# Performance work log

Measured on AMD Instinct MI355X. Metric: run time of the kernel, lower is better.

Reference implementation:

```python
import jax, jax.numpy as jnp
import numpy as np

N = 50000          # nodes
E = 800000         # edges (before self loops)
F_IN = 16
HID = 64
HEADS = 4
C = 64             # per-head out channels (concat=False)
G = 64             # graphs in batch
NEG_SLOPE = 0.2


def setup_inputs() -> dict:
    key = jax.random.key(0)
    ks = jax.random.split(key, 20)
    inp = {
        "x": jax.random.normal(ks[0], (N, F_IN), jnp.float32),
        "edge_index": jax.random.randint(ks[1], (2, E), 0, N, jnp.int64),
        "batch": jnp.sort(jax.random.randint(ks[2], (N,), 0, G, jnp.int64)),
        "W_in": jax.random.normal(ks[3], (HID, F_IN), jnp.float32) * 0.1,
        "b_in": jnp.zeros((HID,), jnp.float32),
        "W_out": jax.random.normal(ks[4], (1, HID), jnp.float32) * 0.1,
        "b_out": jnp.zeros((1,), jnp.float32),
    }
    for l in range(3):
        inp[f"W{l}"] = jax.random.normal(ks[5 + 4 * l], (HEADS * C, HID), jnp.float32) * 0.1
        inp[f"asrc{l}"] = jax.random.normal(ks[6 + 4 * l], (HEADS, C), jnp.float32) * 0.1
        inp[f"adst{l}"] = jax.random.normal(ks[7 + 4 * l], (HEADS, C), jnp.float32) * 0.1
        inp[f"bg{l}"] = jnp.zeros((HID,), jnp.float32)
    return inp


def _gat_layer(x, W, a_src, a_dst, bias, src, dst, n):
    # x: [N, HID] -> h: [N, HEADS, C]
    h = (x @ W.T).reshape(n, HEADS, C)
    alpha_s = jnp.einsum("nhc,hc->nh", h, a_src)   # [N, H]
    alpha_d = jnp.einsum("nhc,hc->nh", h, a_dst)
    e = jax.nn.leaky_relu(alpha_s[src] + alpha_d[dst], NEG_SLOPE)  # [E', H]
    # segment softmax over incoming edges of each dst node
    m = jax.ops.segment_max(e, dst, num_segments=n)
    e = jnp.exp(e - m[dst])
    s = jax.ops.segment_sum(e, dst, num_segments=n)
    alpha = e / (s[dst] + 1e-16)                                   # [E', H]
    msg = alpha[:, :, None] * h[src]                               # [E', H, C]
    out = jax.ops.segment_sum(msg, dst, num_segments=n)            # [N, H, C]
    return out.mean(axis=1) + bias                                 # concat=False: head mean


def reference(x, W_in, b_in, W0, asrc0, adst0, bg0, W1, asrc1, adst1, bg1,
              W2, asrc2, adst2, bg2, W_out, b_out, edge_index, batch):
    n = x.shape[0]
    # add self loops (PyG GATConv default)
    loops = jnp.arange(n, dtype=edge_index.dtype)
    src = jnp.concatenate([edge_index[0], loops])
    dst = jnp.concatenate([edge_index[1], loops])

    h = x @ W_in.T + b_in
    for W, a_s, a_d, bg in ((W0, asrc0, adst0, bg0),
                            (W1, asrc1, adst1, bg1),
                            (W2, asrc2, adst2, bg2)):
        h = jax.nn.relu(_gat_layer(h, W, a_s, a_d, bg, src, dst, n))
        # dropout p=0.2 is inactive in eval mode

    # global mean pool over graphs
    sums = jax.ops.segment_sum(h, batch, num_segments=G)
    cnt = jax.ops.segment_sum(jnp.ones((n,), h.dtype), batch, num_segments=G)
    graph_emb = sums / jnp.maximum(cnt, 1.0)[:, None]              # [G, HID]

    return jax.nn.sigmoid(graph_emb @ W_out.T + b_out)             # [G, 1]
```

## Files before the change

kernel.cpp:

```cpp
#include <hip/hip_runtime.h>
#include <hip/hip_bf16.h>
#include <hip/hip_fp16.h>

#define HID 64
#define HEADS 4
#define GCNT 64
#define F_IN 16
#define NEG 0.2f
#define NBUCK 256
#define BSLOT 6144
#define SCHUNK 2048
#define BSTRIDE 16

typedef _Float16 f16x8 __attribute__((ext_vector_type(8)));
typedef float f32x4 __attribute__((ext_vector_type(4)));

__device__ __forceinline__ unsigned pack_h2(float a, float b) {
  __half2 h = __floats2half2_rn(a, b);
  union { __half2 h; unsigned u; } c;
  c.h = h;
  return c.u;
}
__device__ __forceinline__ __half2 uas_h2(unsigned u) {
  union { unsigned u; __half2 h; } c;
  c.u = u;
  return c.h;
}
__device__ __forceinline__ unsigned h2_as_u(__half2 h) {
  union { __half2 h; unsigned u; } c;
  c.h = h;
  return c.u;
}
__device__ __forceinline__ __half2 xor16_add(__half2 v) {
  unsigned u = (unsigned)__shfl_xor((int)h2_as_u(v), 16, 64);
  return __hadd2(v, uas_h2(u));
}

__global__ __launch_bounds__(256) void k_pre(
    const float* __restrict__ W0, const float* __restrict__ asrc,
    const float* __restrict__ adst, const float* __restrict__ Win,
    const float* __restrict__ bin, int* __restrict__ bcur,
    float* __restrict__ vb, float* __restrict__ c8) {
  int t = threadIdx.x;
  if (blockIdx.x == 0) {
    for (int i = t; i < NBUCK * BSTRIDE; i += 256) bcur[i] = 0;
    return;
  }
  __shared__ float vaL[512];
#pragma unroll
  for (int it = 0; it < 2; ++it) {
    int idx = t + it * 256;
    int q = idx >> 6, j = idx & 63;
    const float* a = (q < 4) ? asrc : adst;
    int h = q & 3;
    float s = 0.f;
    for (int c = 0; c < 64; ++c) s += a[h * 64 + c] * W0[(h * 64 + c) * 64 + j];
    vaL[idx] = s;
  }
  __syncthreads();
  if (t < 128) {
    int q = t >> 4, k = t & 15;
    float s = 0.f;
    for (int j = 0; j < 64; ++j) s += vaL[q * 64 + j] * Win[j * F_IN + k];
    vb[t] = s;
  } else if (t < 136) {
    int q = t - 128;
    float s = 0.f;
    for (int j = 0; j < 64; ++j) s += vaL[q * 64 + j] * bin[j];
    c8[q] = s;
  }
}

__global__ __launch_bounds__(256) void k_binit(
    const int* __restrict__ ei, int* __restrict__ bcur,
    unsigned* __restrict__ tmp, int E, int N,
    const float* __restrict__ x, const float* __restrict__ Win,
    const float* __restrict__ bin,
    const float* __restrict__ W0, const float* __restrict__ W1,
    const float* __restrict__ W2,
    __half* __restrict__ Wh3, __half* __restrict__ Wcat3,
    float* __restrict__ sums, const float* __restrict__ vb,
    const float* __restrict__ c8,
    float* __restrict__ as_, float* __restrict__ ad_,
    __half* __restrict__ hh, int BUK) {
  int t = threadIdx.x;
  if (blockIdx.x < BUK) {
    __shared__ int hist[NBUCK];
    __shared__ int base[NBUCK];
    int start = blockIdx.x * SCHUNK;
    int end = min(start + SCHUNK, E + N);
    hist[t] = 0;
    __syncthreads();
    unsigned val[8];
    int rank[8];
    bool ok[8];
#pragma unroll
    for (int k = 0; k < 8; ++k) {
      int i = start + t + k * 256;
      ok[k] = i < end;
      if (ok[k]) {
        int s, d;
        if (i < E) {
          s = ei[i];
          d = ei[E + i];
        } else {
          s = d = i - E;
        }
        val[k] = ((unsigned)d << 16) | (unsigned)s;
        rank[k] = atomicAdd(&hist[d >> 8], 1);
      }
    }
    __syncthreads();
    int h = hist[t];
    base[t] = h ? atomicAdd(&bcur[t * BSTRIDE], h) : 0;
    __syncthreads();
#pragma unroll
    for (int k = 0; k < 8; ++k) {
      if (ok[k]) {
        int bk = (int)(val[k] >> 24);
        int idx = base[bk] + rank[k];
        if (idx < BSLOT) tmp[(size_t)bk * BSLOT + idx] = val[k];
      }
    }
    return;
  }
  int b = blockIdx.x - BUK;
  if (b < 384) {
    int i = b * 256 + t;
    if (i < 49152) {
      const float* W = (i < 16384) ? W0 : (i < 32768) ? W1 : W2;
      Wh3[i] = __float2half(W[i & 16383]);
    } else {
      int j = i - 49152;
      int l = j >> 14;
      int r = j & 16383;
      int c = r >> 8;
      int k256 = r & 255;
      int h = k256 & 3, kk = k256 >> 2;
      const float* W = (l == 0) ? W0 : (l == 1) ? W1 : W2;
      Wcat3[j] = __float2half(0.25f * W[(h * 64 + c) * 64 + kk]);
    }
    return;
  }
  if (b < 401) {
    int i = (b - 384) * 256 + t;
    if (i < GCNT * HID + GCNT) sums[i] = 0.f;
    return;
  }
  {
    __shared__ float Ws[1024];
    __shared__ float vbs[128];
    __shared__ float bins[64];
    __shared__ float c8s[8];
    for (int i = t; i < 1024; i += 256) Ws[i] = Win[i];
    if (t < 128) vbs[t] = vb[t];
    if (t < 64) bins[t] = bin[t];
    if (t < 8) c8s[t] = c8[t];
    __syncthreads();
    int b2 = b - 401;
    int n = b2 * 64 + (t >> 2);
    int p = t & 3;
    if (n >= N) return;
    const float4* xr4 = (const float4*)(x + (size_t)n * F_IN);
    float4 a0 = xr4[0], a1 = xr4[1], a2 = xr4[2], a3 = xr4[3];
    float xv[16] = {a0.x, a0.y, a0.z, a0.w, a1.x, a1.y, a1.z, a1.w,
                    a2.x, a2.y, a2.z, a2.w, a3.x, a3.y, a3.z, a3.w};
    unsigned hv[8];
#pragma unroll
    for (int jj = 0; jj < 16; jj += 2) {
      int j = p * 16 + jj;
      float acc0 = bins[j], acc1 = bins[j + 1];
#pragma unroll
      for (int k = 0; k < 16; ++k) {
        acc0 = fmaf(xv[k], Ws[j * 16 + k], acc0);
        acc1 = fmaf(xv[k], Ws[(j + 1) * 16 + k], acc1);
      }
      hv[jj >> 1] = pack_h2(acc0, acc1);
    }
    uint4* dst = (uint4*)(hh + (size_t)n * 64 + p * 16);
    dst[0] = make_uint4(hv[0], hv[1], hv[2], hv[3]);
    dst[1] = make_uint4(hv[4], hv[5], hv[6], hv[7]);
    if (p == 0) {
      float sq[8];
#pragma unroll
      for (int q = 0; q < 8; ++q) {
        float s = c8s[q];
#pragma unroll
        for (int k = 0; k < 16; ++k) s = fmaf(xv[k], vbs[q * 16 + k], s);
        sq[q] = s;
      }
      *(float4*)(as_ + (size_t)n * 4) = make_float4(sq[0], sq[1], sq[2], sq[3]);
      *(float4*)(ad_ + (size_t)n * 4) = make_float4(sq[4], sq[5], sq[6], sq[7]);
    }
  }
}

__global__ __launch_bounds__(256) void k_bsort(
    const unsigned* __restrict__ tmp, const int* __restrict__ bcur,
    int* __restrict__ rowptr, int* __restrict__ col, int N) {
  __shared__ int s[NBUCK];
  __shared__ int hist[NBUCK];
  __shared__ int pref[NBUCK];
  int b = blockIdx.x, t = threadIdx.x;
  int c = min(bcur[t * BSTRIDE], BSLOT);
  s[t] = c;
  __syncthreads();
  for (int o = 1; o < 256; o <<= 1) {
    int x = (t >= o) ? s[t - o] : 0;
    __syncthreads();
    s[t] += x;
    __syncthreads();
  }
  int base = (b == 0) ? 0 : s[b - 1];
  int total = s[255];
  int cntb = min(bcur[b * BSTRIDE], BSLOT);
  hist[t] = 0;
  __syncthreads();
  for (int j = t; j < cntb; j += 256)
    atomicAdd(&hist[(tmp[(size_t)b * BSLOT + j] >> 16) & 255], 1);
  __syncthreads();
  int v = hist[t];
  pref[t] = v;
  __syncthreads();
  for (int o = 1; o < 256; o <<= 1) {
    int x = (t >= o) ? pref[t - o] : 0;
    __syncthreads();
    pref[t] += x;
    __syncthreads();
  }
  pref[t] -= v;
  __syncthreads();
  int node = b * 256 + t;
  if (node < N) rowptr[node] = base + pref[t];
  if (b == 255 && t == 255) rowptr[N] = total;
  hist[t] = 0;
  __syncthreads();
  for (int j = t; j < cntb; j += 256) {
    unsigned e = tmp[(size_t)b * BSLOT + j];
    int d8 = (int)((e >> 16) & 255);
    int r = atomicAdd(&hist[d8], 1);
    col[base + pref[d8] + r] = (int)(e & 0xffffu);
  }
}

__device__ __forceinline__ void gat_one_node(
    int node, int lane, const __half* __restrict__ h, const float* __restrict__ as_,
    const float* __restrict__ ad_, const int* __restrict__ rowptr,
    const int* __restrict__ col, __half* __restrict__ Mrow) {
  int r0 = rowptr[node];
  int deg = rowptr[node + 1] - r0;
  float4 adv = *(const float4*)(ad_ + (size_t)node * 4);

  if (deg <= 64) {
    int off = 0;
    float x0 = 0.f, x1 = 0.f, x2 = 0.f, x3 = 0.f;
    if (lane < deg) {
      int s = col[r0 + lane];
      off = s << 6;
      float4 av = *(const float4*)(as_ + (size_t)s * 4);
      float e0 = av.x + adv.x; e0 = (e0 > 0.f) ? e0 : NEG * e0;
      float e1 = av.y + adv.y; e1 = (e1 > 0.f) ? e1 : NEG * e1;
      float e2 = av.z + adv.z; e2 = (e2 > 0.f) ? e2 : NEG * e2;
      float e3 = av.w + adv.w; e3 = (e3 > 0.f) ? e3 : NEG * e3;
      x0 = __expf(fminf(e0, 60.f));
      x1 = __expf(fminf(e1, 60.f));
      x2 = __expf(fminf(e2, 60.f));
      x3 = __expf(fminf(e3, 60.f));
    }
    float s0 = x0, s1 = x1, s2 = x2, s3 = x3;
#pragma unroll
    for (int o = 32; o; o >>= 1) {
      s0 += __shfl_xor(s0, o, 64);
      s1 += __shfl_xor(s1, o, 64);
      s2 += __shfl_xor(s2, o, 64);
      s3 += __shfl_xor(s3, o, 64);
    }
    unsigned w01 = pack_h2(x0 / (s0 + 1e-16f), x1 / (s1 + 1e-16f));
    unsigned w23 = pack_h2(x2 / (s2 + 1e-16f), x3 / (s3 + 1e-16f));
    __half2 acc01 = __floats2half2_rn(0.f, 0.f);
    __half2 acc23 = acc01;
#pragma unroll 4
    for (int j = 0; j < deg; ++j) {
      int oj = __builtin_amdgcn_readlane(off, j) + lane;
      unsigned W01 = __builtin_amdgcn_readlane(w01, j);
      unsigned W23 = __builtin_amdgcn_readlane(w23, j);
      __half2 hv = __half2half2(h[oj]);
      acc01 = __hfma2(hv, uas_h2(W01), acc01);
      acc23 = __hfma2(hv, uas_h2(W23), acc23);
    }
    *(__half2*)&Mrow[lane * 4] = acc01;
    *(__half2*)&Mrow[lane * 4 + 2] = acc23;
    return;
  }
  float m0 = -1e30f, m1 = -1e30f, m2 = -1e30f, m3 = -1e30f;
  for (int j = lane; j < deg; j += 64) {
    int s = col[r0 + j];
    float4 av = *(const float4*)(as_ + (size_t)s * 4);
    float e0 = av.x + adv.x; e0 = (e0 > 0.f) ? e0 : NEG * e0; m0 = fmaxf(m0, e0);
    float e1 = av.y + adv.y; e1 = (e1 > 0.f) ? e1 : NEG * e1; m1 = fmaxf(m1, e1);
    float e2 = av.z + adv.z; e2 = (e2 > 0.f) ? e2 : NEG * e2; m2 = fmaxf(m2, e2);
    float e3 = av.w + adv.w; e3 = (e3 > 0.f) ? e3 : NEG * e3; m3 = fmaxf(m3, e3);
  }
#pragma unroll
  for (int o = 32; o; o >>= 1) {
    m0 = fmaxf(m0, __shfl_xor(m0, o, 64));
    m1 = fmaxf(m1, __shfl_xor(m1, o, 64));
    m2 = fmaxf(m2, __shfl_xor(m2, o, 64));
    m3 = fmaxf(m3, __shfl_xor(m3, o, 64));
  }
  float s0 = 0.f, s1 = 0.f, s2 = 0.f, s3 = 0.f;
  for (int j = lane; j < deg; j += 64) {
    int s = col[r0 + j];
    float4 av = *(const float4*)(as_ + (size_t)s * 4);
    float e0 = av.x + adv.x; e0 = (e0 > 0.f) ? e0 : NEG * e0; s0 += __expf(e0 - m0);
    float e1 = av.y + adv.y; e1 = (e1 > 0.f) ? e1 : NEG * e1; s1 += __expf(e1 - m1);
    float e2 = av.z + adv.z; e2 = (e2 > 0.f) ? e2 : NEG * e2; s2 += __expf(e2 - m2);
    float e3 = av.w + adv.w; e3 = (e3 > 0.f) ? e3 : NEG * e3; s3 += __expf(e3 - m3);
  }
#pragma unroll
  for (int o = 32; o; o >>= 1) {
    s0 += __shfl_xor(s0, o, 64);
    s1 += __shfl_xor(s1, o, 64);
    s2 += __shfl_xor(s2, o, 64);
    s3 += __shfl_xor(s3, o, 64);
  }
  float i0 = 1.f / (s0 + 1e-16f), i1 = 1.f / (s1 + 1e-16f);
  float i2 = 1.f / (s2 + 1e-16f), i3 = 1.f / (s3 + 1e-16f);
  float a0 = 0.f, a1 = 0.f, a2 = 0.f, a3 = 0.f;
  for (int j = 0; j < deg; ++j) {
    int s = col[r0 + j];
    float4 av = *(const float4*)(as_ + (size_t)s * 4);
    float e0 = av.x + adv.x; e0 = (e0 > 0.f) ? e0 : NEG * e0;
    float e1 = av.y + adv.y; e1 = (e1 > 0.f) ? e1 : NEG * e1;
    float e2 = av.z + adv.z; e2 = (e2 > 0.f) ? e2 : NEG * e2;
    float e3 = av.w + adv.w; e3 = (e3 > 0.f) ? e3 : NEG * e3;
    float hv = __half2float(h[(s << 6) + lane]);
    a0 = fmaf(__expf(e0 - m0) * i0, hv, a0);
    a1 = fmaf(__expf(e1 - m1) * i1, hv, a1);
    a2 = fmaf(__expf(e2 - m2) * i2, hv, a2);
    a3 = fmaf(__expf(e3 - m3) * i3, hv, a3);
  }
  *(__half2*)&Mrow[lane * 4] = __floats2half2_rn(a0, a1);
  *(__half2*)&Mrow[lane * 4 + 2] = __floats2half2_rn(a2, a3);
}

__device__ __forceinline__ void gat_pair(
    int pr, int lane, int half, int l5, int N,
    const __half* __restrict__ h, const float* __restrict__ as_,
    const float* __restrict__ ad_, const int* __restrict__ rowptr,
    const int* __restrict__ col, __half* __restrict__ Mt) {
  int n0 = pr * 2;
  int n1 = min(n0 + 1, N - 1);
  int mynode = half ? n1 : n0;
  int r0 = rowptr[mynode];
  int dg = rowptr[mynode + 1] - r0;
  int dgA = __builtin_amdgcn_readlane(dg, 0);
  int dgB = __builtin_amdgcn_readlane(dg, 32);

  if (dgA <= 32 && dgB <= 32) {
    float4 adv = *(const float4*)(ad_ + (size_t)mynode * 4);
    int off = 0;
    float x0 = 0.f, x1 = 0.f, x2 = 0.f, x3 = 0.f;
    if (l5 < dg) {
      int s = col[r0 + l5];
      off = s << 6;
      float4 av = *(const float4*)(as_ + (size_t)s * 4);
      float e0 = av.x + adv.x; e0 = (e0 > 0.f) ? e0 : NEG * e0;
      float e1 = av.y + adv.y; e1 = (e1 > 0.f) ? e1 : NEG * e1;
      float e2 = av.z + adv.z; e2 = (e2 > 0.f) ? e2 : NEG * e2;
      float e3 = av.w + adv.w; e3 = (e3 > 0.f) ? e3 : NEG * e3;
      x0 = __expf(fminf(e0, 60.f));
      x1 = __expf(fminf(e1, 60.f));
      x2 = __expf(fminf(e2, 60.f));
      x3 = __expf(fminf(e3, 60.f));
    }
    float s0 = x0, s1 = x1, s2 = x2, s3 = x3;
#pragma unroll
    for (int o = 16; o; o >>= 1) {
      s0 += __shfl_xor(s0, o, 64);
      s1 += __shfl_xor(s1, o, 64);
      s2 += __shfl_xor(s2, o, 64);
      s3 += __shfl_xor(s3, o, 64);
    }
    unsigned w01 = pack_h2(x0 / (s0 + 1e-16f), x1 / (s1 + 1e-16f));
    unsigned w23 = pack_h2(x2 / (s2 + 1e-16f), x3 / (s3 + 1e-16f));

    int g = l5 >> 4, li = l5 & 15;
    const uint2* h4p = (const uint2*)h;
    __half2 z = __floats2half2_rn(0.f, 0.f);
    __half2 a0_01 = z, a0_23 = z, a1_01 = z, a1_23 = z;
    __half2 a2_01 = z, a2_23 = z, a3_01 = z, a3_23 = z;
    int mdeg = max(dgA, dgB);
    int baddr = half << 7;
#pragma unroll 2
    for (int j = 0; j < mdeg; j += 2) {
      int addr = baddr + (j + g) * 4;
      int oj = __builtin_amdgcn_ds_bpermute(addr, off);
      unsigned W01 = (unsigned)__builtin_amdgcn_ds_bpermute(addr, (int)w01);
      unsigned W23 = (unsigned)__builtin_amdgcn_ds_bpermute(addr, (int)w23);
      uint2 hv = h4p[(oj >> 2) + li];
      __half2 ha = uas_h2(hv.x), hb = uas_h2(hv.y);
      __half2 wA = uas_h2(W01), wB = uas_h2(W23);
      __half2 c0 = __low2half2(ha), c1 = __high2half2(ha);
      __half2 c2 = __low2half2(hb), c3 = __high2half2(hb);
      a0_01 = __hfma2(c0, wA, a0_01); a0_23 = __hfma2(c0, wB, a0_23);
      a1_01 = __hfma2(c1, wA, a1_01); a1_23 = __hfma2(c1, wB, a1_23);
      a2_01 = __hfma2(c2, wA, a2_01); a2_23 = __hfma2(c2, wB, a2_23);
      a3_01 = __hfma2(c3, wA, a3_01); a3_23 = __hfma2(c3, wB, a3_23);
    }
    a0_01 = xor16_add(a0_01); a0_23 = xor16_add(a0_23);
    a1_01 = xor16_add(a1_01); a1_23 = xor16_add(a1_23);
    a2_01 = xor16_add(a2_01); a2_23 = xor16_add(a2_23);
    a3_01 = xor16_add(a3_01); a3_23 = xor16_add(a3_23);
    if (g == 0) {
      __half* row = &Mt[(mynode & 15) * 264 + li * 16];
      uint4 st1, st2;
      st1.x = h2_as_u(a0_01); st1.y = h2_as_u(a0_23);
      st1.z = h2_as_u(a1_01); st1.w = h2_as_u(a1_23);
      st2.x = h2_as_u(a2_01); st2.y = h2_as_u(a2_23);
      st2.z = h2_as_u(a3_01); st2.w = h2_as_u(a3_23);
      *(uint4*)&row[0] = st1;
      *(uint4*)&row[8] = st2;
    }
  } else {
    gat_one_node(n0, lane, h, as_, ad_, rowptr, col, &Mt[(n0 & 15) * 264]);
    if (n1 != n0) gat_one_node(n1, lane, h, as_, ad_, rowptr, col, &Mt[(n1 & 15) * 264]);
  }
}

template <bool FIN>
__global__ __launch_bounds__(256) void k_gatf(
    const __half* __restrict__ h, const float* __restrict__ as_,
    const float* __restrict__ ad_, const int* __restrict__ rowptr,
    const int* __restrict__ col, const __half* __restrict__ Wcat,
    const float* __restrict__ bg, const __half* __restrict__ Wn,
    const float* __restrict__ asrc, const float* __restrict__ adst,
    __half* __restrict__ hout, float* __restrict__ nas, float* __restrict__ nad,
    const int* __restrict__ batchv, float* __restrict__ gsums,
    int N) {
  __shared__ __half Mt[16 * 264];
  __shared__ __half O[16 * 72];
  int tid = threadIdx.x;
  int lane = tid & 63, wv = tid >> 6;
  int tile = blockIdx.x;
  int half = lane >> 5, l5 = lane & 31;
  int npairs = (N + 1) >> 1;

  int pr0 = tile * 8 + wv * 2;
  int pr1 = pr0 + 1;
  bool has0 = pr0 < npairs, has1 = pr1 < npairs;
  if (has0 && has1) {
    int my0 = min(pr0 * 2 + half, N - 1);
    int my1 = min(pr1 * 2 + half, N - 1);
    int r0a = rowptr[my0];
    int dga = rowptr[my0 + 1] - r0a;
    int r0b = rowptr[my1];
    int dgb = rowptr[my1 + 1] - r0b;
    int dA0 = __builtin_amdgcn_readlane(dga, 0);
    int dB0 = __builtin_amdgcn_readlane(dga, 32);
    int dA1 = __builtin_amdgcn_readlane(dgb, 0);
    int dB1 = __builtin_amdgcn_readlane(dgb, 32);

    if (dA0 <= 32 && dB0 <= 32 && dA1 <= 32 && dB1 <= 32) {
      float4 adva = *(const float4*)(ad_ + (size_t)my0 * 4);
      float4 advb = *(const float4*)(ad_ + (size_t)my1 * 4);
      int offa = 0, offb = 0;
      float xa0 = 0.f, xa1 = 0.f, xa2 = 0.f, xa3 = 0.f;
      float xb0 = 0.f, xb1 = 0.f, xb2 = 0.f, xb3 = 0.f;
      if (l5 < dga) {
        int s = col[r0a + l5];
        offa = s << 6;
        float4 av = *(const float4*)(as_ + (size_t)s * 4);
        float e0 = av.x + adva.x; e0 = (e0 > 0.f) ? e0 : NEG * e0;
        float e1 = av.y + adva.y; e1 = (e1 > 0.f) ? e1 : NEG * e1;
        float e2 = av.z + adva.z; e2 = (e2 > 0.f) ? e2 : NEG * e2;
        float e3 = av.w + adva.w; e3 = (e3 > 0.f) ? e3 : NEG * e3;
        xa0 = __expf(fminf(e0, 60.f));
        xa1 = __expf(fminf(e1, 60.f));
        xa2 = __expf(fminf(e2, 60.f));
        xa3 = __expf(fminf(e3, 60.f));
      }
      if (l5 < dgb) {
        int s = col[r0b + l5];
        offb = s << 6;
        float4 av = *(const float4*)(as_ + (size_t)s * 4);
        float e0 = av.x + advb.x; e0 = (e0 > 0.f) ? e0 : NEG * e0;
        float e1 = av.y + advb.y; e1 = (e1 > 0.f) ? e1 : NEG * e1;
        float e2 = av.z + advb.z; e2 = (e2 > 0.f) ? e2 : NEG * e2;
        float e3 = av.w + advb.w; e3 = (e3 > 0.f) ? e3 : NEG * e3;
        xb0 = __expf(fminf(e0, 60.f));
        xb1 = __expf(fminf(e1, 60.f));
        xb2 = __expf(fminf(e2, 60.f));
        xb3 = __expf(fminf(e3, 60.f));
      }
      float sa0 = xa0, sa1 = xa1, sa2 = xa2, sa3 = xa3;
      float sb0 = xb0, sb1 = xb1, sb2 = xb2, sb3 = xb3;
#pragma unroll
      for (int o = 16; o; o >>= 1) {
        sa0 += __shfl_xor(sa0, o, 64);
        sa1 += __shfl_xor(sa1, o, 64);
        sa2 += __shfl_xor(sa2, o, 64);
        sa3 += __shfl_xor(sa3, o, 64);
        sb0 += __shfl_xor(sb0, o, 64);
        sb1 += __shfl_xor(sb1, o, 64);
        sb2 += __shfl_xor(sb2, o, 64);
        sb3 += __shfl_xor(sb3, o, 64);
      }
      unsigned w01a = pack_h2(xa0 / (sa0 + 1e-16f), xa1 / (sa1 + 1e-16f));
      unsigned w23a = pack_h2(xa2 / (sa2 + 1e-16f), xa3 / (sa3 + 1e-16f));
      unsigned w01b = pack_h2(xb0 / (sb0 + 1e-16f), xb1 / (sb1 + 1e-16f));
      unsigned w23b = pack_h2(xb2 / (sb2 + 1e-16f), xb3 / (sb3 + 1e-16f));

      uint4* EB = (uint4*)&Mt[wv * 1056];
      EB[half * 32 + l5] = make_uint4((unsigned)offa, w01a, w23a, 0u);
      EB[64 + half * 32 + l5] = make_uint4((unsigned)offb, w01b, w23b, 0u);

      int g = l5 >> 4, li = l5 & 15;
      const uint2* h4p = (const uint2*)h;
      __half2 z = __floats2half2_rn(0.f, 0.f);
      __half2 pa0 = z, pa1 = z, pa2 = z, pa3 = z, pa4 = z, pa5 = z, pa6 = z, pa7 = z;
      __half2 pb0 = z, pb1 = z, pb2 = z, pb3 = z, pb4 = z, pb5 = z, pb6 = z, pb7 = z;
      int mm = max(max(dA0, dB0), max(dA1, dB1));
      int ebase = half * 32;
#pragma unroll 2
      for (int j = 0; j < mm; j += 2) {
        uint4 ra = EB[ebase + j + g];
        uint4 rb = EB[64 + ebase + j + g];
        uint2 hva = h4p[((int)ra.x >> 2) + li];
        uint2 hvb = h4p[((int)rb.x >> 2) + li];
        {
          __half2 ha = uas_h2(hva.x), hb = uas_h2(hva.y);
          __half2 wA = uas_h2(ra.y), wB = uas_h2(ra.z);
          __half2 c0 = __low2half2(ha), c1 = __high2half2(ha);
          __half2 c2 = __low2half2(hb), c3 = __high2half2(hb);
          pa0 = __hfma2(c0, wA, pa0); pa1 = __hfma2(c0, wB, pa1);
          pa2 = __hfma2(c1, wA, pa2); pa3 = __hfma2(c1, wB, pa3);
          pa4 = __hfma2(c2, wA, pa4); pa5 = __hfma2(c2, wB, pa5);
          pa6 = __hfma2(c3, wA, pa6); pa7 = __hfma2(c3, wB, pa7);
        }
        {
          __half2 ha = uas_h2(hvb.x), hb = uas_h2(hvb.y);
          __half2 wA = uas_h2(rb.y), wB = uas_h2(rb.z);
          __half2 c0 = __low2half2(ha), c1 = __high2half2(ha);
          __half2 c2 = __low2half2(hb), c3 = __high2half2(hb);
          pb0 = __hfma2(c0, wA, pb0); pb1 = __hfma2(c0, wB, pb1);
          pb2 = __hfma2(c1, wA, pb2); pb3 = __hfma2(c1, wB, pb3);
          pb4 = __hfma2(c2, wA, pb4); pb5 = __hfma2(c2, wB, pb5);
          pb6 = __hfma2(c3, wA, pb6); pb7 = __hfma2(c3, wB, pb7);
        }
      }
      pa0 = xor16_add(pa0); pa1 = xor16_add(pa1); pa2 = xor16_add(pa2); pa3 = xor16_add(pa3);
      pa4 = xor16_add(pa4); pa5 = xor16_add(pa5); pa6 = xor16_add(pa6); pa7 = xor16_add(pa7);
      pb0 = xor16_add(pb0); pb1 = xor16_add(pb1); pb2 = xor16_add(pb2); pb3 = xor16_add(pb3);
      pb4 = xor16_add(pb4); pb5 = xor16_add(pb5); pb6 = xor16_add(pb6); pb7 = xor16_add(pb7);
      if (g == 0) {
        __half* rowA = &Mt[(my0 & 15) * 264 + li * 16];
        __half* rowB = &Mt[(my1 & 15) * 264 + li * 16];
        uint4 s1, s2;
        s1.x = h2_as_u(pa0); s1.y = h2_as_u(pa1); s1.z = h2_as_u(pa2); s1.w = h2_as_u(pa3);
        s2.x = h2_as_u(pa4); s2.y = h2_as_u(pa5); s2.z = h2_as_u(pa6); s2.w = h2_as_u(pa7);
        *(uint4*)&rowA[0] = s1;
        *(uint4*)&rowA[8] = s2;
        s1.x = h2_as_u(pb0); s1.y = h2_as_u(pb1); s1.z = h2_as_u(pb2); s1.w = h2_as_u(pb3);
        s2.x = h2_as_u(pb4); s2.y = h2_as_u(pb5); s2.z = h2_as_u(pb6); s2.w = h2_as_u(pb7);
        *(uint4*)&rowB[0] = s1;
        *(uint4*)&rowB[8] = s2;
      }
    } else {
      gat_pair(pr0, lane, half, l5, N, h, as_, ad_, rowptr, col, Mt);
      gat_pair(pr1, lane, half, l5, N, h, as_, ad_, rowptr, col, Mt);
    }
  } else if (has0) {
    gat_pair(pr0, lane, half, l5, N, h, as_, ad_, rowptr, col, Mt);
  }
  __syncthreads();

  int quad = lane >> 4, n16 = lane & 15;
  const f16x8* WC = (const f16x8*)Wcat;
  int ch1 = wv * 16 + n16;
  float bias1 = bg[ch1];
  f32x4 c1 = {0.f, 0.f, 0.f, 0.f};
#pragma unroll
  for (int i = 0; i < 8; ++i) {
    f16x8 a = *(const f16x8*)&Mt[n16 * 264 + (i * 4 + quad) * 8];
    c1 = __builtin_amdgcn_mfma_f32_16x16x32_f16(a, WC[ch1 * 32 + i * 4 + quad], c1, 0, 0, 0);
  }
#pragma unroll
  for (int r = 0; r < 4; ++r) {
    float v = fmaxf(c1[r] + bias1, 0.f);
    O[(quad * 4 + r) * 72 + ch1] = __float2half(v);
  }
  __syncthreads();

  if (FIN) {
    if (tid < 64) {
      float* cnt_ = gsums + GCNT * HID;
      int c = tid;
      int nmax = min(16, N - tile * 16);
      int curg = -1;
      float acc = 0.f;
      int cacc = 0;
      for (int i = 0; i < nmax; ++i) {
        int gph = batchv[tile * 16 + i];
        float v = __half2float(O[i * 72 + c]);
        if (gph != curg) {
          if (curg >= 0) {
            atomicAdd(&gsums[curg * HID + c], acc);
            if (c == 0) atomicAdd(&cnt_[curg], (float)cacc);
          }
          curg = gph;
          acc = 0.f;
          cacc = 0;
        }
        acc += v;
        ++cacc;
      }
      if (curg >= 0) {
        atomicAdd(&gsums[curg * HID + c], acc);
        if (c == 0) atomicAdd(&cnt_[curg], (float)cacc);
      }
    }
    return;
  }

  {
    int nd = tid >> 4, c0 = (tid & 15) * 4;
    int node = tile * 16 + nd;
    if (node < N) {
      uint2 v = *(const uint2*)&O[nd * 72 + c0];
      *(uint2*)&hout[(size_t)node * 64 + c0] = v;
    }
  }
  {
    const f16x8* WN = (const f16x8*)Wn;
    f16x8 a0 = *(const f16x8*)&O[n16 * 72 + quad * 8];
    f16x8 a1 = *(const f16x8*)&O[n16 * 72 + 32 + quad * 8];
    f32x4 accs[4];
#pragma unroll
    for (int nt = 0; nt < 4; ++nt) {
      int ch = wv * 64 + nt * 16 + n16;
      f32x4 zz = {0.f, 0.f, 0.f, 0.f};
      zz = __builtin_amdgcn_mfma_f32_16x16x32_f16(a0, WN[ch * 8 + quad], zz, 0, 0, 0);
      zz = __builtin_amdgcn_mfma_f32_16x16x32_f16(a1, WN[ch * 8 + 4 + quad], zz, 0, 0, 0);
      accs[nt] = zz;
    }
#pragma unroll
    for (int r = 0; r < 4; ++r) {
      float vs = 0.f, vd = 0.f;
#pragma unroll
      for (int nt = 0; nt < 4; ++nt) {
        int ch = wv * 64 + nt * 16 + n16;
        vs = fmaf(accs[nt][r], asrc[ch], vs);
        vd = fmaf(accs[nt][r], adst[ch], vd);
      }
#pragma unroll
      for (int o = 8; o; o >>= 1) {
        vs += __shfl_xor(vs, o, 64);
        vd += __shfl_xor(vd, o, 64);
      }
      int node = tile * 16 + quad * 4 + r;
      if (n16 == 0 && node < N) {
        nas[(size_t)node * 4 + wv] = vs;
        nad[(size_t)node * 4 + wv] = vd;
      }
    }
  }
}

__global__ void k_out(const float* __restrict__ sums, const float* __restrict__ cnt,
                      const float* __restrict__ Wout, const float* __restrict__ bout,
                      float* __restrict__ out) {
  int g = blockIdx.x, lane = threadIdx.x;
  float cg = fmaxf(cnt[g], 1.f);
  float v = (sums[g * HID + lane] / cg) * Wout[lane];
#pragma unroll
  for (int o = 32; o; o >>= 1) v += __shfl_xor(v, o, 64);
  if (lane == 0) out[g] = 1.f / (1.f + __expf(-v));
}

extern "C" void kernel_launch(void* const* d_in, const int* in_sizes, int n_in,
                              void* d_out, int out_size, void* d_ws, size_t ws_size,
                              hipStream_t stream) {
  const float* x    = (const float*)d_in[0];
  const int*   ei   = (const int*)d_in[1];
  const int*   batch= (const int*)d_in[2];
  const float* Win  = (const float*)d_in[3];
  const float* bin  = (const float*)d_in[4];
  const float* Wout = (const float*)d_in[5];
  const float* bout = (const float*)d_in[6];
  const float* Wl[3]    = {(const float*)d_in[7],  (const float*)d_in[11], (const float*)d_in[15]};
  const float* asrcl[3] = {(const float*)d_in[8],  (const float*)d_in[12], (const float*)d_in[16]};
  const float* adstl[3] = {(const float*)d_in[9],  (const float*)d_in[13], (const float*)d_in[17]};
  const float* bgl[3]   = {(const float*)d_in[10], (const float*)d_in[14], (const float*)d_in[18]};

  int N = in_sizes[2];
  int E = in_sizes[1] / 2;
  int EE = E + N;

  char* p = (char*)d_ws;
  auto alloc = [&](size_t bytes) {
    char* r = p;
    p += (bytes + 255) & ~(size_t)255;
    return r;
  };
  int*      rowptr = (int*)alloc((size_t)(N + 1) * 4);
  int*      col    = (int*)alloc((size_t)EE * 4);
  unsigned* tmp    = (unsigned*)alloc((size_t)NBUCK * BSLOT * 4);
  int*      bcur   = (int*)alloc((size_t)NBUCK * BSTRIDE * 4);
  float*    vb     = (float*)alloc(128 * 4);
  float*    c8     = (float*)alloc(8 * 4);
  __half*   hhA    = (__half*)alloc((size_t)N * HID * 2);
  __half*   hhB    = (__half*)alloc((size_t)N * HID * 2);
  float*    asA    = (float*)alloc((size_t)N * HEADS * 4);
  float*    adA    = (float*)alloc((size_t)N * HEADS * 4);
  float*    asB    = (float*)alloc((size_t)N * HEADS * 4);
  float*    adB    = (float*)alloc((size_t)N * HEADS * 4);
  __half*   Wh3    = (__half*)alloc(3 * 16384 * 2);
  __half*   Wcat3  = (__half*)alloc(3 * 16384 * 2);
  float*    sums   = (float*)alloc((size_t)(GCNT * HID + GCNT) * 4);
  float*    cnt    = sums + GCNT * HID;

  int tiles = (N + 15) / 16;
  int BUK = (EE + SCHUNK - 1) / SCHUNK;
  int initB = 401 + (N + 63) / 64;

  k_pre<<<2, 256, 0, stream>>>(Wl[0], asrcl[0], adstl[0], Win, bin, bcur, vb, c8);

  k_binit<<<BUK + initB, 256, 0, stream>>>(ei, bcur, tmp, E, N,
                                           x, Win, bin, Wl[0], Wl[1], Wl[2],
                                           Wh3, Wcat3, sums, vb, c8, asA, adA, hhA, BUK);

  k_bsort<<<NBUCK, 256, 0, stream>>>(tmp, bcur, rowptr, col, N);

  k_gatf<false><<<tiles, 256, 0, stream>>>(hhA, asA, adA, rowptr, col,
                                           Wcat3, bgl[0], Wh3 + 16384, asrcl[1], adstl[1],
                                           hhB, asB, adB, nullptr, nullptr, N);
  k_gatf<false><<<tiles, 256, 0, stream>>>(hhB, asB, adB, rowptr, col,
                                           Wcat3 + 16384, bgl[1], Wh3 + 32768, asrcl[2], adstl[2],
                                           hhA, asA, adA, nullptr, nullptr, N);
  k_gatf<true><<<tiles, 256, 0, stream>>>(hhA, asA, adA, rowptr, col,
                                          Wcat3 + 32768, bgl[2], nullptr, nullptr, nullptr,
                                          nullptr, nullptr, nullptr, batch, sums, N);

  k_out<<<GCNT, 64, 0, stream>>>(sums, cnt, Wout, bout, (float*)d_out);
}
```

Baseline: 295.7 us.

## Use 512-thread blocks with one node pair per wave in GAT aggregation

The fused GAT layer kernel now launches 8 waves per block instead of 4. Each wave handles one node pair instead of two, so the same 16-node tile is spread across twice as many waves. The per-wave edge loop now walks two edges per step into two separate accumulator sets, which keeps memory-level parallelism while lowering register use per wave. The MFMA projection and output stages run only in the first 256 threads, so half the block sits idle during those phases and there is extra barrier cost.

```diff
diff --git a/kernel.cpp b/kernel.cpp
--- a/kernel.cpp
+++ b/kernel.cpp
@@ -35,6 +35,18 @@
   unsigned u = (unsigned)__shfl_xor((int)h2_as_u(v), 16, 64);
   return __hadd2(v, uas_h2(u));
 }
+
+#define FMA_REC(HV, W01, W23, P0, P1, P2, P3, P4, P5, P6, P7)      \
+  do {                                                             \
+    __half2 _ha = uas_h2((HV).x), _hb = uas_h2((HV).y);            \
+    __half2 _wA = uas_h2(W01), _wB = uas_h2(W23);                  \
+    __half2 _c0 = __low2half2(_ha), _c1 = __high2half2(_ha);       \
+    __half2 _c2 = __low2half2(_hb), _c3 = __high2half2(_hb);       \
+    P0 = __hfma2(_c0, _wA, P0); P1 = __hfma2(_c0, _wB, P1);        \
+    P2 = __hfma2(_c1, _wA, P2); P3 = __hfma2(_c1, _wB, P3);        \
+    P4 = __hfma2(_c2, _wA, P4); P5 = __hfma2(_c2, _wB, P5);        \
+    P6 = __hfma2(_c3, _wA, P6); P7 = __hfma2(_c3, _wB, P7);        \
+  } while (0)
 
 __global__ __launch_bounds__(256) void k_pre(
     const float* __restrict__ W0, const float* __restrict__ asrc,
@@ -429,7 +441,7 @@
 }
 
 template <bool FIN>
-__global__ __launch_bounds__(256) void k_gatf(
+__global__ __launch_bounds__(512) void k_gatf(
     const __half* __restrict__ h, const float* __restrict__ as_,
     const float* __restrict__ ad_, const int* __restrict__ rowptr,
     const int* __restrict__ col, const __half* __restrict__ Wcat,
@@ -446,149 +458,99 @@
   int half = lane >> 5, l5 = lane & 31;
   int npairs = (N + 1) >> 1;
 
-  int pr0 = tile * 8 + wv * 2;
-  int pr1 = pr0 + 1;
-  bool has0 = pr0 < npairs, has1 = pr1 < npairs;
-  if (has0 && has1) {
-    int my0 = min(pr0 * 2 + half, N - 1);
-    int my1 = min(pr1 * 2 + half, N - 1);
-    int r0a = rowptr[my0];
-    int dga = rowptr[my0 + 1] - r0a;
-    int r0b = rowptr[my1];
-    int dgb = rowptr[my1 + 1] - r0b;
-    int dA0 = __builtin_amdgcn_readlane(dga, 0);
-    int dB0 = __builtin_amdgcn_readlane(dga, 32);
-    int dA1 = __builtin_amdgcn_readlane(dgb, 0);
-    int dB1 = __builtin_amdgcn_readlane(dgb, 32);
-
-    if (dA0 <= 32 && dB0 <= 32 && dA1 <= 32 && dB1 <= 32) {
-      float4 adva = *(const float4*)(ad_ + (size_t)my0 * 4);
-      float4 advb = *(const float4*)(ad_ + (size_t)my1 * 4);
-      int offa = 0, offb = 0;
-      float xa0 = 0.f, xa1 = 0.f, xa2 = 0.f, xa3 = 0.f;
-      float xb0 = 0.f, xb1 = 0.f, xb2 = 0.f, xb3 = 0.f;
-      if (l5 < dga) {
-        int s = col[r0a + l5];
-        offa = s << 6;
+  int pr = tile * 8 + wv;
+  if (pr < npairs) {
+    int n0 = pr * 2;
+    int n1 = min(n0 + 1, N - 1);
+    int mynode = half ? n1 : n0;
+    int r0 = rowptr[mynode];
+    int dg = rowptr[mynode + 1] - r0;
+    int dgA = __builtin_amdgcn_readlane(dg, 0);
+    int dgB = __builtin_amdgcn_readlane(dg, 32);
+
+    if (dgA <= 32 && dgB <= 32) {
+      float4 adv = *(const float4*)(ad_ + (size_t)mynode * 4);
+      int off = 0;
+      float x0 = 0.f, x1 = 0.f, x2 = 0.f, x3 = 0.f;
+      if (l5 < dg) {
+        int s = col[r0 + l5];
+        off = s << 6;
         float4 av = *(const float4*)(as_ + (size_t)s * 4);
-        float e0 = av.x + adva.x; e0 = (e0 > 0.f) ? e0 : NEG * e0;
-        float e1 = av.y + adva.y; e1 = (e1 > 0.f) ? e1 : NEG * e1;
-        float e2 = av.z + adva.z; e2 = (e2 > 0.f) ? e2 : NEG * e2;
-        float e3 = av.w + adva.w; e3 = (e3 > 0.f) ? e3 : NEG * e3;
-        xa0 = __expf(fminf(e0, 60.f));
-        xa1 = __expf(fminf(e1, 60.f));
-        xa2 = __expf(fminf(e2, 60.f));
-        xa3 = __expf(fminf(e3, 60.f));
-      }
-      if (l5 < dgb) {
-        int s = col[r0b + l5];
-        offb = s << 6;
-        float4 av = *(const float4*)(as_ + (size_t)s * 4);
-        float e0 = av.x + advb.x; e0 = (e0 > 0.f) ? e0 : NEG * e0;
-        float e1 = av.y + advb.y; e1 = (e1 > 0.f) ? e1 : NEG * e1;
-        float e2 = av.z + advb.z; e2 = (e2 > 0.f) ? e2 : NEG * e2;
-        float e3 = av.w + advb.w; e3 = (e3 > 0.f) ? e3 : NEG * e3;
-        xb0 = __expf(fminf(e0, 60.f));
-        xb1 = __expf(fminf(e1, 60.f));
-        xb2 = __expf(fminf(e2, 60.f));
-        xb3 = __expf(fminf(e3, 60.f));
-      }
-      float sa0 = xa0, sa1 = xa1, sa2 = xa2, sa3 = xa3;
-      float sb0 = xb0, sb1 = xb1, sb2 = xb2, sb3 = xb3;
+        float e0 = av.x + adv.x; e0 = (e0 > 0.f) ? e0 : NEG * e0;
+        float e1 = av.y + adv.y; e1 = (e1 > 0.f) ? e1 : NEG * e1;
+        float e2 = av.z + adv.z; e2 = (e2 > 0.f) ? e2 : NEG * e2;
+        float e3 = av.w + adv.w; e3 = (e3 > 0.f) ? e3 : NEG * e3;
+        x0 = __expf(fminf(e0, 60.f));
+        x1 = __expf(fminf(e1, 60.f));
+        x2 = __expf(fminf(e2, 60.f));
+        x3 = __expf(fminf(e3, 60.f));
+      }
+      float s0 = x0, s1 = x1, s2 = x2, s3 = x3;
 #pragma unroll
       for (int o = 16; o; o >>= 1) {
-        sa0 += __shfl_xor(sa0, o, 64);
-        sa1 += __shfl_xor(sa1, o, 64);
-        sa2 += __shfl_xor(sa2, o, 64);
-        sa3 += __shfl_xor(sa3, o, 64);
-        sb0 += __shfl_xor(sb0, o, 64);
-        sb1 += __shfl_xor(sb1, o, 64);
-        sb2 += __shfl_xor(sb2, o, 64);
-        sb3 += __shfl_xor(sb3, o, 64);
-      }
-      unsigned w01a = pack_h2(xa0 / (sa0 + 1e-16f), xa1 / (sa1 + 1e-16f));
-      unsigned w23a = pack_h2(xa2 / (sa2 + 1e-16f), xa3 / (sa3 + 1e-16f));
-      unsigned w01b = pack_h2(xb0 / (sb0 + 1e-16f), xb1 / (sb1 + 1e-16f));
-      unsigned w23b = pack_h2(xb2 / (sb2 + 1e-16f), xb3 / (sb3 + 1e-16f));
-
-      uint4* EB = (uint4*)&Mt[wv * 1056];
-      EB[half * 32 + l5] = make_uint4((unsigned)offa, w01a, w23a, 0u);
-      EB[64 + half * 32 + l5] = make_uint4((unsigned)offb, w01b, w23b, 0u);
-
+        s0 += __shfl_xor(s0, o, 64);
+        s1 += __shfl_xor(s1, o, 64);
+        s2 += __shfl_xor(s2, o, 64);
+        s3 += __shfl_xor(s3, o, 64);
+      }
+      unsigned w01 = pack_h2(x0 / (s0 + 1e-16f), x1 / (s1 + 1e-16f));
+      unsigned w23 = pack_h2(x2 / (s2 + 1e-16f), x3 / (s3 + 1e-16f));
+
+      uint4* EB = (uint4*)&Mt[wv * 528];
+      EB[half * 32 + l5] = make_uint4((unsigned)off, w01, w23, 0u);
+
+      int mdeg = max(dgA, dgB);
       int g = l5 >> 4, li = l5 & 15;
+      int eH = half * 32;
       const uint2* h4p = (const uint2*)h;
       __half2 z = __floats2half2_rn(0.f, 0.f);
       __half2 pa0 = z, pa1 = z, pa2 = z, pa3 = z, pa4 = z, pa5 = z, pa6 = z, pa7 = z;
-      __half2 pb0 = z, pb1 = z, pb2 = z, pb3 = z, pb4 = z, pb5 = z, pb6 = z, pb7 = z;
-      int mm = max(max(dA0, dB0), max(dA1, dB1));
-      int ebase = half * 32;
+      __half2 qa0 = z, qa1 = z, qa2 = z, qa3 = z, qa4 = z, qa5 = z, qa6 = z, qa7 = z;
 #pragma unroll 2
-      for (int j = 0; j < mm; j += 2) {
-        uint4 ra = EB[ebase + j + g];
-        uint4 rb = EB[64 + ebase + j + g];
+      for (int j = 0; j < mdeg; j += 4) {
+        uint4 ra = EB[eH + j + g];
+        uint4 rb = EB[eH + j + 2 + g];
         uint2 hva = h4p[((int)ra.x >> 2) + li];
         uint2 hvb = h4p[((int)rb.x >> 2) + li];
-        {
-          __half2 ha = uas_h2(hva.x), hb = uas_h2(hva.y);
-          __half2 wA = uas_h2(ra.y), wB = uas_h2(ra.z);
-          __half2 c0 = __low2half2(ha), c1 = __high2half2(ha);
-          __half2 c2 = __low2half2(hb), c3 = __high2half2(hb);
-          pa0 = __hfma2(c0, wA, pa0); pa1 = __hfma2(c0, wB, pa1);
-          pa2 = __hfma2(c1, wA, pa2); pa3 = __hfma2(c1, wB, pa3);
-          pa4 = __hfma2(c2, wA, pa4); pa5 = __hfma2(c2, wB, pa5);
-          pa6 = __hfma2(c3, wA, pa6); pa7 = __hfma2(c3, wB, pa7);
-        }
-        {
-          __half2 ha = uas_h2(hvb.x), hb = uas_h2(hvb.y);
-          __half2 wA = uas_h2(rb.y), wB = uas_h2(rb.z);
-          __half2 c0 = __low2half2(ha), c1 = __high2half2(ha);
-          __half2 c2 = __low2half2(hb), c3 = __high2half2(hb);
-          pb0 = __hfma2(c0, wA, pb0); pb1 = __hfma2(c0, wB, pb1);
-          pb2 = __hfma2(c1, wA, pb2); pb3 = __hfma2(c1, wB, pb3);
-          pb4 = __hfma2(c2, wA, pb4); pb5 = __hfma2(c2, wB, pb5);
-          pb6 = __hfma2(c3, wA, pb6); pb7 = __hfma2(c3, wB, pb7);
-        }
-      }
+        FMA_REC(hva, ra.y, ra.z, pa0, pa1, pa2, pa3, pa4, pa5, pa6, pa7);
+        FMA_REC(hvb, rb.y, rb.z, qa0, qa1, qa2, qa3, qa4, qa5, qa6, qa7);
+      }
+      pa0 = __hadd2(pa0, qa0); pa1 = __hadd2(pa1, qa1);
+      pa2 = __hadd2(pa2, qa2); pa3 = __hadd2(pa3, qa3);
+      pa4 = __hadd2(pa4, qa4); pa5 = __hadd2(pa5, qa5);
+      pa6 = __hadd2(pa6, qa6); pa7 = __hadd2(pa7, qa7);
       pa0 = xor16_add(pa0); pa1 = xor16_add(pa1); pa2 = xor16_add(pa2); pa3 = xor16_add(pa3);
       pa4 = xor16_add(pa4); pa5 = xor16_add(pa5); pa6 = xor16_add(pa6); pa7 = xor16_add(pa7);
-      pb0 = xor16_add(pb0); pb1 = xor16_add(pb1); pb2 = xor16_add(pb2); pb3 = xor16_add(pb3);
-      pb4 = xor16_add(pb4); pb5 = xor16_add(pb5); pb6 = xor16_add(pb6); pb7 = xor16_add(pb7);
       if (g == 0) {
-        __half* rowA = &Mt[(my0 & 15) * 264 + li * 16];
-        __half* rowB = &Mt[(my1 & 15) * 264 + li * 16];
-        uint4 s1, s2;
-        s1.x = h2_as_u(pa0); s1.y = h2_as_u(pa1); s1.z = h2_as_u(pa2); s1.w = h2_as_u(pa3);
-        s2.x = h2_as_u(pa4); s2.y = h2_as_u(pa5); s2.z = h2_as_u(pa6); s2.w = h2_as_u(pa7);
-        *(uint4*)&rowA[0] = s1;
-        *(uint4*)&rowA[8] = s2;
-        s1.x = h2_as_u(pb0); s1.y = h2_as_u(pb1); s1.z = h2_as_u(pb2); s1.w = h2_as_u(pb3);
-        s2.x = h2_as_u(pb4); s2.y = h2_as_u(pb5); s2.z = h2_as_u(pb6); s2.w = h2_as_u(pb7);
-        *(uint4*)&rowB[0] = s1;
-        *(uint4*)&rowB[8] = s2;
+        __half* row = &Mt[(mynode & 15) * 264 + li * 16];
+        uint4 s1v, s2v;
+        s1v.x = h2_as_u(pa0); s1v.y = h2_as_u(pa1); s1v.z = h2_as_u(pa2); s1v.w = h2_as_u(pa3);
+        s2v.x = h2_as_u(pa4); s2v.y = h2_as_u(pa5); s2v.z = h2_as_u(pa6); s2v.w = h2_as_u(pa7);
+        *(uint4*)&row[0] = s1v;
+        *(uint4*)&row[8] = s2v;
       }
     } else {
-      gat_pair(pr0, lane, half, l5, N, h, as_, ad_, rowptr, col, Mt);
-      gat_pair(pr1, lane, half, l5, N, h, as_, ad_, rowptr, col, Mt);
-    }
-  } else if (has0) {
-    gat_pair(pr0, lane, half, l5, N, h, as_, ad_, rowptr, col, Mt);
+      gat_pair(pr, lane, half, l5, N, h, as_, ad_, rowptr, col, Mt);
+    }
   }
   __syncthreads();
 
   int quad = lane >> 4, n16 = lane & 15;
-  const f16x8* WC = (const f16x8*)Wcat;
   int ch1 = wv * 16 + n16;
-  float bias1 = bg[ch1];
-  f32x4 c1 = {0.f, 0.f, 0.f, 0.f};
-#pragma unroll
-  for (int i = 0; i < 8; ++i) {
-    f16x8 a = *(const f16x8*)&Mt[n16 * 264 + (i * 4 + quad) * 8];
-    c1 = __builtin_amdgcn_mfma_f32_16x16x32_f16(a, WC[ch1 * 32 + i * 4 + quad], c1, 0, 0, 0);
-  }
-#pragma unroll
-  for (int r = 0; r < 4; ++r) {
-    float v = fmaxf(c1[r] + bias1, 0.f);
-    O[(quad * 4 + r) * 72 + ch1] = __float2half(v);
+  if (tid < 256) {
+    const f16x8* WC = (const f16x8*)Wcat;
+    float bias1 = bg[ch1];
+    f32x4 c1 = {0.f, 0.f, 0.f, 0.f};
+#pragma unroll
+    for (int i = 0; i < 8; ++i) {
+      f16x8 a = *(const f16x8*)&Mt[n16 * 264 + (i * 4 + quad) * 8];
+      c1 = __builtin_amdgcn_mfma_f32_16x16x32_f16(a, WC[ch1 * 32 + i * 4 + quad], c1, 0, 0, 0);
+    }
+#pragma unroll
+    for (int r = 0; r < 4; ++r) {
+      float v = fmaxf(c1[r] + bias1, 0.f);
+      O[(quad * 4 + r) * 72 + ch1] = __float2half(v);
+    }
   }
   __syncthreads();
 
@@ -623,15 +585,15 @@
     return;
   }
 
-  {
-    int nd = tid >> 4, c0 = (tid & 15) * 4;
-    int node = tile * 16 + nd;
-    if (node < N) {
-      uint2 v = *(const uint2*)&O[nd * 72 + c0];
-      *(uint2*)&hout[(size_t)node * 64 + c0] = v;
-    }
-  }
-  {
+  if (tid < 256) {
+    {
+      int nd = tid >> 4, c0 = (tid & 15) * 4;
+      int node = tile * 16 + nd;
+      if (node < N) {
+        uint2 v = *(const uint2*)&O[nd * 72 + c0];
+        *(uint2*)&hout[(size_t)node * 64 + c0] = v;
+      }
+    }
     const f16x8* WN = (const f16x8*)Wn;
     f16x8 a0 = *(const f16x8*)&O[n16 * 72 + quad * 8];
     f16x8 a1 = *(const f16x8*)&O[n16 * 72 + 32 + quad * 8];
@@ -732,13 +694,13 @@
 
   k_bsort<<<NBUCK, 256, 0, stream>>>(tmp, bcur, rowptr, col, N);
 
-  k_gatf<false><<<tiles, 256, 0, stream>>>(hhA, asA, adA, rowptr, col,
+  k_gatf<false><<<tiles, 512, 0, stream>>>(hhA, asA, adA, rowptr, col,
                                            Wcat3, bgl[0], Wh3 + 16384, asrcl[1], adstl[1],
                                            hhB, asB, adB, nullptr, nullptr, N);
-  k_gatf<false><<<tiles, 256, 0, stream>>>(hhB, asB, adB, rowptr, col,
+  k_gatf<false><<<tiles, 512, 0, stream>>>(hhB, asB, adB, rowptr, col,
                                            Wcat3 + 16384, bgl[1], Wh3 + 32768, asrcl[2], adstl[2],
                                            hhA, asA, adA, nullptr, nullptr, N);
-  k_gatf<true><<<tiles, 256, 0, stream>>>(hhA, asA, adA, rowptr, col,
+  k_gatf<true><<<tiles, 512, 0, stream>>>(hhA, asA, adA, rowptr, col,
                                           Wcat3 + 32768, bgl[2], nullptr, nullptr, nullptr,
                                           nullptr, nullptr, nullptr, batch, sums, N);
 
```

Result: faster. 289.1 us (-2.2%).
